# Kernel tuning notes

Hardware: AMD Instinct MI355X
Metric: run time of the kernel (lower is better)

## Reference

```python
import jax, jax.numpy as jnp
import numpy as np
from jax import lax

V, E, H, D = 50000, 300, 128, 128   # vocab, embed, gru_units, dense_units
B, S, W, T = 32, 512, 20, 16        # batch, sentences/doc, words/sentence, topics/doc


def setup_inputs() -> dict:
    key = jax.random.key(0)
    ks = jax.random.split(key, 16)
    word_ids = jax.random.randint(ks[0], (B, S, W), 0, V, dtype=jnp.int32)
    # contiguous equal topic segments, 1-based inclusive boundaries
    L = S // T
    starts = (1 + np.arange(T) * L).astype(np.int32)
    ends = (starts + L - 1).astype(np.int32)
    topic_start_ends = jnp.asarray(np.broadcast_to(np.stack([starts, ends], -1), (B, T, 2)))
    sc = 0.05
    def rn(k, shape, s=sc):
        return jax.random.normal(k, shape, dtype=jnp.float32) * s
    inp = {
        "word_ids": word_ids,
        "topic_start_ends": topic_start_ends,
        "emb": rn(ks[1], (V, E), 0.6),
        "Wih_f": rn(ks[2], (3 * H, E)), "Whh_f": rn(ks[3], (3 * H, H)),
        "bih_f": rn(ks[4], (3 * H,)),   "bhh_f": rn(ks[5], (3 * H,)),
        "Wih_b": rn(ks[6], (3 * H, E)), "Whh_b": rn(ks[7], (3 * H, H)),
        "bih_b": rn(ks[8], (3 * H,)),   "bhh_b": rn(ks[9], (3 * H,)),
        "W_att": rn(ks[10], (4 * H, 4 * H)), "v_att": rn(ks[11], (4 * H, 1)),
        "W1": rn(ks[12], (D, 4 * H)), "b1": rn(ks[13], (D,)),
        "W2": rn(ks[14], (1, D)),     "b2": rn(ks[15], (1,)),
    }
    return inp


def _gru_dir(x_sbe, Wih, Whh, bih, bhh, reverse):
    """x_sbe: [S,B,E] -> (outputs [S,B,H] in original time order, last hidden [B,H])."""
    h0 = jnp.zeros((x_sbe.shape[1], Whh.shape[1]), x_sbe.dtype)
    def step(h, xt):
        gx = xt @ Wih.T + bih            # [B,3H]
        gh = h @ Whh.T + bhh
        xr, xz, xn = jnp.split(gx, 3, axis=-1)   # PyTorch gate order: r,z,n
        hr, hz, hn = jnp.split(gh, 3, axis=-1)
        r = jax.nn.sigmoid(xr + hr)
        z = jax.nn.sigmoid(xz + hz)
        n = jnp.tanh(xn + r * hn)
        h2 = (1.0 - z) * n + z * h
        return h2, h2
    last, outs = lax.scan(step, h0, x_sbe, reverse=reverse)
    return outs, last


def reference(word_ids, topic_start_ends, emb,
              Wih_f, Whh_f, bih_f, bhh_f,
              Wih_b, Whh_b, bih_b, bhh_b,
              W_att, v_att, W1, b1, W2, b2):
    # --- sent_encoder: mean word embedding per sentence ---
    x = jnp.mean(emb[word_ids], axis=2)              # [B,S,E]
    # --- doc_encoder: biGRU over sentences ---
    xs = jnp.swapaxes(x, 0, 1)                       # [S,B,E]
    out_f, last_f = _gru_dir(xs, Wih_f, Whh_f, bih_f, bhh_f, reverse=False)
    out_b, last_b = _gru_dir(xs, Wih_b, Whh_b, bih_b, bhh_b, reverse=True)
    sent_rep = jnp.swapaxes(jnp.concatenate([out_f, out_b], axis=-1), 0, 1)  # [B,S,2H]
    # faithful to torch hidden.view(B, 2H) on [2,B,H] contiguous memory
    doc_vec = jnp.stack([last_f, last_b], axis=0).reshape(sent_rep.shape[0], 2 * last_f.shape[1])
    doc_rep = jnp.broadcast_to(doc_vec[:, None, :], sent_rep.shape)          # [B,S,2H]
    # --- topic segment extraction via boundary diffs on zero-padded GRU out ---
    Bn, Sn, twoH = sent_rep.shape
    Hn = twoH // 2
    P = jnp.pad(sent_rep, ((0, 0), (1, 1), (0, 0)))   # [B,S+2,2H]; index i = 1-based sentence i
    starts = topic_start_ends[..., 0]                 # [B,T], 1-based
    ends = topic_start_ends[..., 1]
    bidx = jnp.arange(Bn)[:, None]
    fw = P[bidx, ends, :Hn] - P[bidx, starts - 1, :Hn]      # forward-dir diff
    bw = P[bidx, starts, Hn:] - P[bidx, ends + 1, Hn:]      # backward-dir diff
    topic_mat = jnp.concatenate([fw, bw], axis=-1)          # [B,T,2H]
    # scatter: sentence s (0-based) belongs to topic with starts-1 <= s <= ends-1
    pos = jnp.arange(Sn, dtype=starts.dtype) + 1            # 1-based sentence ids
    seg = jax.vmap(lambda st: jnp.searchsorted(st, pos, side='right') - 1)(starts)  # [B,S]
    topic_rep = jnp.take_along_axis(topic_mat, seg[..., None], axis=1)              # [B,S,2H]
    # --- decoder ---
    cat_ds = jnp.concatenate([doc_rep, sent_rep], axis=-1)   # [B,S,4H]
    cat_ts = jnp.concatenate([topic_rep, sent_rep], axis=-1)
    doc_scores = jnp.tanh(cat_ds @ W_att) @ v_att            # [B,S,1]
    topic_scores = jnp.tanh(cat_ts @ W_att) @ v_att
    ssum = doc_scores + topic_scores
    context = (doc_scores / ssum) * doc_rep + (topic_scores / ssum) * topic_rep
    inp = jnp.concatenate([sent_rep, context], axis=-1)      # [B,S,4H]
    h = jax.nn.relu(inp @ W1.T + b1)                         # dropout = identity (eval)
    logits = h @ W2.T + b2                                   # [B,S,1]
    return logits
```

## Files before the change

kernel.cpp:

```cpp
#include <hip/hip_runtime.h>
#include <hip/hip_bf16.h>

#define B_ 32
#define S_ 512
#define W_ 20
#define T_ 16
#define E_ 300
#define H_ 128
#define M_ (B_*S_)

typedef float f32x4 __attribute__((ext_vector_type(4)));

#define OFF_GX        0ul
#define OFF_X         12582912ul
#define OFF_SENT      17498112ul
#define OFF_LASTF     21692416ul
#define OFF_LASTB     21696512ul
#define OFF_DOCVEC    21700608ul
#define OFF_TOPICMAT  21708800ul
#define OFF_DOCPART   21839872ul
#define OFF_TOPICPART 21856256ul
#define OFF_SEG       22118400ul
#define OFF_WTIH      22134784ul
#define OFF_BIASIH    22365184ul
#define OFF_W1T       22365952ul
#define OFF_H         22431488ul
#define OFF_SRPART    0ul
#define OFF_CTX       OFF_X

__global__ void prep_kernel(const float* __restrict__ Wih_f, const float* __restrict__ Wih_b,
                            const float* __restrict__ bih_f, const float* __restrict__ bih_b,
                            const float* __restrict__ W1,
                            float* __restrict__ Wt_ih, float* __restrict__ bias_ih,
                            float* __restrict__ W1t) {
  int idx = blockIdx.x * 256 + threadIdx.x;
  if (idx < E_ * 768) {
    int k = idx / 768, g = idx % 768;
    Wt_ih[idx] = (g < 384) ? Wih_f[g * E_ + k] : Wih_b[(g - 384) * E_ + k];
  }
  if (idx < 768) bias_ih[idx] = (idx < 384) ? bih_f[idx] : bih_b[idx - 384];
  if (idx < 512 * 128) { int k = idx / 128, j = idx % 128; W1t[idx] = W1[j * 512 + k]; }
}

__global__ void embed_mean_kernel(const int* __restrict__ wid, const float* __restrict__ emb,
                                  float* __restrict__ x) {
  int m = blockIdx.x;
  const int* ids = wid + (size_t)m * W_;
  int e = threadIdx.x;
  float s0 = 0.f, s1 = 0.f, s2 = 0.f;
  for (int w = 0; w < W_; w++) {
    const float* row = emb + (size_t)ids[w] * E_;
    s0 += row[e];
    s1 += row[e + 128];
    if (e < E_ - 256) s2 += row[e + 256];
  }
  const float inv = 1.0f / (float)W_;
  float* xr = x + (size_t)m * E_;
  xr[e] = s0 * inv; xr[e + 128] = s1 * inv; if (e < E_ - 256) xr[e + 256] = s2 * inv;
}

template<bool BIAS, bool ACCUM, bool RELU>
__global__ __launch_bounds__(256) void gemm64(
    const float* __restrict__ A, int lda,
    const float* __restrict__ B, int ldb,
    float* __restrict__ C, int ldc,
    const float* __restrict__ bias,
    int M, int N, int K) {
  __shared__ float As[16][68];
  __shared__ float Bs[16][68];
  const int tid = threadIdx.x;
  const int n0 = blockIdx.x * 64, m0 = blockIdx.y * 64;
  const int tx = tid & 15, ty = tid >> 4;
  const int am = tid >> 2, ak = (tid & 3) << 2;
  const int bk = tid >> 4, bn = (tid & 15) << 2;
  float acc[4][4] = {};
  for (int k0 = 0; k0 < K; k0 += 16) {
    float4 av = make_float4(0.f, 0.f, 0.f, 0.f);
    int arow = m0 + am;
    if (arow < M) {
      if (k0 + ak + 3 < K) {
        av = *(const float4*)(A + (size_t)arow * lda + k0 + ak);
      } else {
        float tmp[4] = {0.f, 0.f, 0.f, 0.f};
        #pragma unroll
        for (int i2 = 0; i2 < 4; i2++) { int k = k0 + ak + i2; if (k < K) tmp[i2] = A[(size_t)arow * lda + k]; }
        av = make_float4(tmp[0], tmp[1], tmp[2], tmp[3]);
      }
    }
    As[ak + 0][am] = av.x; As[ak + 1][am] = av.y; As[ak + 2][am] = av.z; As[ak + 3][am] = av.w;
    float4 bv = make_float4(0.f, 0.f, 0.f, 0.f);
    {
      int k = k0 + bk;
      if (k < K) bv = *(const float4*)(B + (size_t)k * ldb + n0 + bn);
    }
    *(float4*)&Bs[bk][bn] = bv;
    __syncthreads();
    #pragma unroll
    for (int kk = 0; kk < 16; kk++) {
      float4 a = *(const float4*)&As[kk][ty << 2];
      float4 b = *(const float4*)&Bs[kk][tx << 2];
      acc[0][0] = fmaf(a.x, b.x, acc[0][0]); acc[0][1] = fmaf(a.x, b.y, acc[0][1]);
      acc[0][2] = fmaf(a.x, b.z, acc[0][2]); acc[0][3] = fmaf(a.x, b.w, acc[0][3]);
      acc[1][0] = fmaf(a.y, b.x, acc[1][0]); acc[1][1] = fmaf(a.y, b.y, acc[1][1]);
      acc[1][2] = fmaf(a.y, b.z, acc[1][2]); acc[1][3] = fmaf(a.y, b.w, acc[1][3]);
      acc[2][0] = fmaf(a.z, b.x, acc[2][0]); acc[2][1] = fmaf(a.z, b.y, acc[2][1]);
      acc[2][2] = fmaf(a.z, b.z, acc[2][2]); acc[2][3] = fmaf(a.z, b.w, acc[2][3]);
      acc[3][0] = fmaf(a.w, b.x, acc[3][0]); acc[3][1] = fmaf(a.w, b.y, acc[3][1]);
      acc[3][2] = fmaf(a.w, b.z, acc[3][2]); acc[3][3] = fmaf(a.w, b.w, acc[3][3]);
    }
    __syncthreads();
  }
  float4 bias4 = make_float4(0.f, 0.f, 0.f, 0.f);
  if (BIAS) bias4 = *(const float4*)(bias + n0 + (tx << 2));
  #pragma unroll
  for (int i = 0; i < 4; i++) {
    int row = m0 + (ty << 2) + i;
    if (row >= M) break;
    float* cp = C + (size_t)row * ldc + n0 + (tx << 2);
    float4 v = make_float4(acc[i][0], acc[i][1], acc[i][2], acc[i][3]);
    if (BIAS) { v.x += bias4.x; v.y += bias4.y; v.z += bias4.z; v.w += bias4.w; }
    if (ACCUM) { float4 o = *(const float4*)cp; v.x += o.x; v.y += o.y; v.z += o.z; v.w += o.w; }
    if (RELU) { v.x = fmaxf(v.x, 0.f); v.y = fmaxf(v.y, 0.f); v.z = fmaxf(v.z, 0.f); v.w = fmaxf(v.w, 0.f); }
    *(float4*)cp = v;
  }
}

#define SWZ(k) ((k) + 4 * ((k) >> 4))

#define AW(N, V) asm volatile("v_accvgpr_write_b32 a" #N ", %0" :: "v"(V) : "a" #N)
#define AWQ(N0, N1, N2, N3, Q) do { AW(N0, (Q).x); AW(N1, (Q).y); AW(N2, (Q).z); AW(N3, (Q).w); } while (0)

#define A96CLOB \
  "a0","a1","a2","a3","a4","a5","a6","a7","a8","a9","a10","a11","a12","a13","a14","a15", \
  "a16","a17","a18","a19","a20","a21","a22","a23","a24","a25","a26","a27","a28","a29","a30","a31", \
  "a32","a33","a34","a35","a36","a37","a38","a39","a40","a41","a42","a43","a44","a45","a46","a47", \
  "a48","a49","a50","a51","a52","a53","a54","a55","a56","a57","a58","a59","a60","a61","a62","a63", \
  "a64","a65","a66","a67","a68","a69","a70","a71","a72","a73","a74","a75","a76","a77","a78","a79", \
  "a80","a81","a82","a83","a84","a85","a86","a87","a88","a89","a90","a91","a92","a93","a94","a95"

#define RD(T, N) "v_accvgpr_read_b32 %[" #T "], a" #N "\n\t"
#define FM(P, T, X) "v_fmac_f32 %[" #P "], %[" #T "], %[" #X "]\n\t"
#define COLA(CR, CZ, CN, X) \
  RD(t0, CR) RD(t1, CZ) RD(t2, CN) FM(pr, t0, X) FM(pz, t1, X) FM(pn, t2, X)

__global__ __launch_bounds__(512, 2) void gru_kernel(
    const float* __restrict__ gxbuf,
    const float* __restrict__ Whh_f, const float* __restrict__ Whh_b,
    const float* __restrict__ bhh_f, const float* __restrict__ bhh_b,
    float* __restrict__ sent_rep,
    float* __restrict__ last_f, float* __restrict__ last_b) {
  const int bid = blockIdx.x;
  const int dir = bid >> 5, b = bid & 31;
  const int t = threadIdx.x;
  const int j = t >> 2;
  const int q = t & 3;
  const int k0 = q << 5;
  const float* Whh = dir ? Whh_b : Whh_f;
  const float* bhh = dir ? bhh_b : bhh_f;

  {
    const float* Wr = Whh + (size_t)j * 128 + k0;
    const float* Wz = Whh + (size_t)(128 + j) * 128 + k0;
    const float* Wn = Whh + (size_t)(256 + j) * 128 + k0;
    f32x4 w0 = *(const f32x4*)(Wr + 0),  w1 = *(const f32x4*)(Wr + 4);
    f32x4 w2 = *(const f32x4*)(Wr + 8),  w3 = *(const f32x4*)(Wr + 12);
    f32x4 w4 = *(const f32x4*)(Wr + 16), w5 = *(const f32x4*)(Wr + 20);
    f32x4 w6 = *(const f32x4*)(Wr + 24), w7 = *(const f32x4*)(Wr + 28);
    AWQ(0, 1, 2, 3, w0);   AWQ(4, 5, 6, 7, w1);   AWQ(8, 9, 10, 11, w2);  AWQ(12, 13, 14, 15, w3);
    AWQ(16, 17, 18, 19, w4); AWQ(20, 21, 22, 23, w5); AWQ(24, 25, 26, 27, w6); AWQ(28, 29, 30, 31, w7);
    w0 = *(const f32x4*)(Wz + 0);  w1 = *(const f32x4*)(Wz + 4);
    w2 = *(const f32x4*)(Wz + 8);  w3 = *(const f32x4*)(Wz + 12);
    w4 = *(const f32x4*)(Wz + 16); w5 = *(const f32x4*)(Wz + 20);
    w6 = *(const f32x4*)(Wz + 24); w7 = *(const f32x4*)(Wz + 28);
    AWQ(32, 33, 34, 35, w0); AWQ(36, 37, 38, 39, w1); AWQ(40, 41, 42, 43, w2); AWQ(44, 45, 46, 47, w3);
    AWQ(48, 49, 50, 51, w4); AWQ(52, 53, 54, 55, w5); AWQ(56, 57, 58, 59, w6); AWQ(60, 61, 62, 63, w7);
    w0 = *(const f32x4*)(Wn + 0);  w1 = *(const f32x4*)(Wn + 4);
    w2 = *(const f32x4*)(Wn + 8);  w3 = *(const f32x4*)(Wn + 12);
    w4 = *(const f32x4*)(Wn + 16); w5 = *(const f32x4*)(Wn + 20);
    w6 = *(const f32x4*)(Wn + 24); w7 = *(const f32x4*)(Wn + 28);
    AWQ(64, 65, 66, 67, w0); AWQ(68, 69, 70, 71, w1); AWQ(72, 73, 74, 75, w2); AWQ(76, 77, 78, 79, w3);
    AWQ(80, 81, 82, 83, w4); AWQ(84, 85, 86, 87, w5); AWQ(88, 89, 90, 91, w6); AWQ(92, 93, 94, 95, w7);
  }

  const float cR = (q == 0) ? bhh[j] : 0.f;
  const float cZ = (q == 0) ? bhh[128 + j] : 0.f;
  const float cN = (q == 0) ? bhh[256 + j] : 0.f;
  const int gate = (q == 1) ? 0 : (q == 2) ? 1 : 2;
  const float mr = (q == 1) ? 1.f : 0.f;
  const float mz = (q == 2) ? 1.f : 0.f;

  __shared__ float lds[320];
  if (t < 128) lds[SWZ(t)] = 0.f;
  __syncthreads();

  const int stp = dir ? -1 : 1;
  const int ts0 = dir ? 511 : 0;
  const ptrdiff_t g768 = (ptrdiff_t)stp * 768;
  const ptrdiff_t s256 = (ptrdiff_t)stp * 256;
  const float* gq = gxbuf + (size_t)b * 512 * 768 + dir * 384 + gate * 128 + j + (size_t)ts0 * 768;
  float* sp = sent_rep + (size_t)b * 512 * 256 + dir * 128 + (size_t)ts0 * 256;
  float hprev = 0.f;
  float gx_c = gq[0];
  float gx_1 = gq[g768];

#define GRU_STEP(P, SOFF) do { \
    float gx_2 = 0.f; \
    if (s + 2 + (SOFF) < 512) gx_2 = gq[2 * g768]; \
    const f32x4* hv = (const f32x4*)(lds + (P) * 160 + 40 * q); \
    f32x4 h0 = hv[0], h1 = hv[1], h2 = hv[2], h3 = hv[3]; \
    f32x4 h4 = hv[5], h5 = hv[6], h6 = hv[7], h7 = hv[8]; \
    float pr = cR, pz = cZ, pn = cN; \
    { float t0v, t1v, t2v; \
      asm volatile( \
        COLA(0,32,64,x0)   COLA(1,33,65,x1)   COLA(2,34,66,x2)   COLA(3,35,67,x3) \
        COLA(4,36,68,x4)   COLA(5,37,69,x5)   COLA(6,38,70,x6)   COLA(7,39,71,x7) \
        COLA(8,40,72,x8)   COLA(9,41,73,x9)   COLA(10,42,74,x10) COLA(11,43,75,x11) \
        COLA(12,44,76,x12) COLA(13,45,77,x13) COLA(14,46,78,x14) COLA(15,47,79,x15) \
        : [pr]"+v"(pr), [pz]"+v"(pz), [pn]"+v"(pn), \
          [t0]"=&v"(t0v), [t1]"=&v"(t1v), [t2]"=&v"(t2v) \
        : [x0]"v"(h0.x), [x1]"v"(h0.y), [x2]"v"(h0.z), [x3]"v"(h0.w), \
          [x4]"v"(h1.x), [x5]"v"(h1.y), [x6]"v"(h1.z), [x7]"v"(h1.w), \
          [x8]"v"(h2.x), [x9]"v"(h2.y), [x10]"v"(h2.z), [x11]"v"(h2.w), \
          [x12]"v"(h3.x), [x13]"v"(h3.y), [x14]"v"(h3.z), [x15]"v"(h3.w) \
        : A96CLOB); \
      asm volatile( \
        COLA(16,48,80,x0)  COLA(17,49,81,x1)  COLA(18,50,82,x2)  COLA(19,51,83,x3) \
        COLA(20,52,84,x4)  COLA(21,53,85,x5)  COLA(22,54,86,x6)  COLA(23,55,87,x7) \
        COLA(24,56,88,x8)  COLA(25,57,89,x9)  COLA(26,58,90,x10) COLA(27,59,91,x11) \
        COLA(28,60,92,x12) COLA(29,61,93,x13) COLA(30,62,94,x14) COLA(31,63,95,x15) \
        : [pr]"+v"(pr), [pz]"+v"(pz), [pn]"+v"(pn), \
          [t0]"=&v"(t0v), [t1]"=&v"(t1v), [t2]"=&v"(t2v) \
        : [x0]"v"(h4.x), [x1]"v"(h4.y), [x2]"v"(h4.z), [x3]"v"(h4.w), \
          [x4]"v"(h5.x), [x5]"v"(h5.y), [x6]"v"(h5.z), [x7]"v"(h5.w), \
          [x8]"v"(h6.x), [x9]"v"(h6.y), [x10]"v"(h6.z), [x11]"v"(h6.w), \
          [x12]"v"(h7.x), [x13]"v"(h7.y), [x14]"v"(h7.z), [x15]"v"(h7.w) \
        : A96CLOB); } \
    pr = fmaf(mr, gx_c, pr); \
    pz = fmaf(mz, gx_c, pz); \
    pr += __shfl_xor(pr, 1); pr += __shfl_xor(pr, 2); \
    pz += __shfl_xor(pz, 1); pz += __shfl_xor(pz, 2); \
    pn += __shfl_xor(pn, 1); pn += __shfl_xor(pn, 2); \
    float xr = fminf(fmaxf(pr, -30.f), 30.f); \
    float xz = fminf(fmaxf(pz, -30.f), 30.f); \
    float r = 1.f / (1.f + __expf(-xr)); \
    float z = 1.f / (1.f + __expf(-xz)); \
    float xn = gx_c + r * pn; xn = fminf(fmaxf(xn, -15.f), 15.f); \
    float e2 = __expf(2.f * xn); \
    float n = (e2 - 1.f) / (e2 + 1.f); \
    float hnew = (1.f - z) * n + z * hprev; \
    hprev = hnew; \
    if (q == 0) { \
      lds[((P) ^ 1) * 160 + SWZ(j)] = hnew; \
      sp[j] = hnew; \
    } \
    __syncthreads(); \
    gq += g768; sp += s256; \
    gx_c = gx_1; gx_1 = gx_2; \
  } while (0)

  #pragma unroll 1
  for (int s = 0; s < 512; s += 2) {
    GRU_STEP(0, 0);
    GRU_STEP(1, 1);
  }
#undef GRU_STEP

  if (q == 0) (dir ? last_b : last_f)[b * 128 + j] = hprev;
}

__global__ void docvec_kernel(const float* __restrict__ last_f, const float* __restrict__ last_b,
                              float* __restrict__ doc_vec) {
  int idx = blockIdx.x * 256 + threadIdx.x;
  int i = idx >> 8, c = idx & 255;
  const float* src = (i < 16) ? last_f : last_b;
  int ii = (i < 16) ? i : i - 16;
  int bb = 2 * ii + (c >> 7);
  doc_vec[idx] = src[bb * 128 + (c & 127)];
}

__global__ void topicmat_kernel(const float* __restrict__ sent_rep, const int* __restrict__ tse,
                                float* __restrict__ topic_mat) {
  int bt = blockIdx.x;
  int b = bt >> 4, t = bt & 15;
  int st = tse[(b * 16 + t) * 2 + 0];
  int en = tse[(b * 16 + t) * 2 + 1];
  int jj = threadIdx.x;
  const float* sr = sent_rep + (size_t)b * 512 * 256;
  float val;
  if (jj < 128) {
    float a = sr[(size_t)(en - 1) * 256 + jj];
    float c = (st - 2 >= 0) ? sr[(size_t)(st - 2) * 256 + jj] : 0.f;
    val = a - c;
  } else {
    float a = sr[(size_t)(st - 1) * 256 + jj];
    float c = (en <= 511) ? sr[(size_t)en * 256 + jj] : 0.f;
    val = a - c;
  }
  topic_mat[(size_t)bt * 256 + jj] = val;
}

__global__ void seg_kernel(const int* __restrict__ tse, int* __restrict__ seg) {
  int idx = blockIdx.x * 256 + threadIdx.x;
  int b = idx >> 9, s = idx & 511;
  int pos = s + 1, cnt = 0;
  for (int t = 0; t < T_; t++) cnt += (tse[(b * T_ + t) * 2] <= pos);
  int sg = cnt - 1; sg = sg < 0 ? 0 : (sg > T_ - 1 ? T_ - 1 : sg);
  seg[idx] = sg;
}

__global__ void scores_ctx_kernel(const float* __restrict__ sr_part,
                                  const float* __restrict__ doc_part,
                                  const float* __restrict__ topic_part,
                                  const float* __restrict__ v_att,
                                  const float* __restrict__ doc_vec,
                                  const float* __restrict__ topic_mat,
                                  const int* __restrict__ seg,
                                  float* __restrict__ context) {
  int wid = threadIdx.x >> 6, lane = threadIdx.x & 63;
  int row = blockIdx.x * 4 + wid;
  int b = row >> 9;
  int sg = seg[row];
  const float* srp = sr_part + (size_t)row * 512;
  const float* dp = doc_part + (size_t)b * 512;
  const float* tp = topic_part + (size_t)(b * 16 + sg) * 512;
  float accd = 0.f, acct = 0.f;
  #pragma unroll
  for (int i = 0; i < 8; i++) {
    int n = lane + i * 64;
    float sp = srp[n], va = v_att[n];
    accd += tanhf(dp[n] + sp) * va;
    acct += tanhf(tp[n] + sp) * va;
  }
  #pragma unroll
  for (int off = 32; off; off >>= 1) { accd += __shfl_xor(accd, off); acct += __shfl_xor(acct, off); }
  float ssum = accd + acct;
  float rd = accd / ssum, rt = acct / ssum;
  const float* dv = doc_vec + (size_t)b * 256;
  const float* tm = topic_mat + (size_t)(b * 16 + sg) * 256;
  float* ctx = context + (size_t)row * 256;
  #pragma unroll
  for (int i = 0; i < 4; i++) {
    int jj = lane + i * 64;
    ctx[jj] = rd * dv[jj] + rt * tm[jj];
  }
}

__global__ void logits_kernel(const float* __restrict__ h, const float* __restrict__ W2,
                              const float* __restrict__ b2, float* __restrict__ out, int M) {
  int wid = threadIdx.x >> 6, lane = threadIdx.x & 63;
  int row = blockIdx.x * 4 + wid;
  if (row >= M) return;
  const float* hp = h + (size_t)row * 128;
  float s = hp[lane] * W2[lane] + hp[lane + 64] * W2[lane + 64];
  #pragma unroll
  for (int off = 32; off; off >>= 1) s += __shfl_xor(s, off);
  if (lane == 0) out[row] = s + b2[0];
}

extern "C" void kernel_launch(void* const* d_in, const int* in_sizes, int n_in,
                              void* d_out, int out_size, void* d_ws, size_t ws_size,
                              hipStream_t stream) {
  const int*   word_ids = (const int*)d_in[0];
  const int*   tse      = (const int*)d_in[1];
  const float* emb      = (const float*)d_in[2];
  const float* Wih_f    = (const float*)d_in[3];
  const float* Whh_f    = (const float*)d_in[4];
  const float* bih_f    = (const float*)d_in[5];
  const float* bhh_f    = (const float*)d_in[6];
  const float* Wih_b    = (const float*)d_in[7];
  const float* Whh_b    = (const float*)d_in[8];
  const float* bih_b    = (const float*)d_in[9];
  const float* bhh_b    = (const float*)d_in[10];
  const float* W_att    = (const float*)d_in[11];
  const float* v_att    = (const float*)d_in[12];
  const float* W1       = (const float*)d_in[13];
  const float* b1       = (const float*)d_in[14];
  const float* W2       = (const float*)d_in[15];
  const float* b2       = (const float*)d_in[16];
  float* ws  = (float*)d_ws;
  float* out = (float*)d_out;

  prep_kernel<<<900, 256, 0, stream>>>(Wih_f, Wih_b, bih_f, bih_b, W1,
                                       ws + OFF_WTIH, ws + OFF_BIASIH, ws + OFF_W1T);
  embed_mean_kernel<<<M_, 128, 0, stream>>>(word_ids, emb, ws + OFF_X);
  gemm64<true, false, false><<<dim3(12, 256), 256, 0, stream>>>(
      ws + OFF_X, E_, ws + OFF_WTIH, 768, ws + OFF_GX, 768, ws + OFF_BIASIH, M_, 768, E_);
  gru_kernel<<<64, 512, 0, stream>>>(ws + OFF_GX, Whh_f, Whh_b, bhh_f, bhh_b,
                                     ws + OFF_SENT, ws + OFF_LASTF, ws + OFF_LASTB);
  docvec_kernel<<<32, 256, 0, stream>>>(ws + OFF_LASTF, ws + OFF_LASTB, ws + OFF_DOCVEC);
  topicmat_kernel<<<512, 256, 0, stream>>>(ws + OFF_SENT, tse, ws + OFF_TOPICMAT);
  seg_kernel<<<64, 256, 0, stream>>>(tse, (int*)(ws + OFF_SEG));
  gemm64<false, false, false><<<dim3(8, 1), 256, 0, stream>>>(
      ws + OFF_DOCVEC, 256, W_att, 512, ws + OFF_DOCPART, 512, nullptr, 32, 512, 256);
  gemm64<false, false, false><<<dim3(8, 8), 256, 0, stream>>>(
      ws + OFF_TOPICMAT, 256, W_att, 512, ws + OFF_TOPICPART, 512, nullptr, 512, 512, 256);
  gemm64<false, false, false><<<dim3(8, 256), 256, 0, stream>>>(
      ws + OFF_SENT, 256, W_att + 256 * 512, 512, ws + OFF_SRPART, 512, nullptr, M_, 512, 256);
  scores_ctx_kernel<<<M_ / 4, 256, 0, stream>>>(
      ws + OFF_SRPART, ws + OFF_DOCPART, ws + OFF_TOPICPART, v_att,
      ws + OFF_DOCVEC, ws + OFF_TOPICMAT, (const int*)(ws + OFF_SEG), ws + OFF_CTX);
  gemm64<true, false, false><<<dim3(2, 256), 256, 0, stream>>>(
      ws + OFF_SENT, 256, ws + OFF_W1T, 128, ws + OFF_H, 128, b1, M_, 128, 256);
  gemm64<false, true, true><<<dim3(2, 256), 256, 0, stream>>>(
      ws + OFF_CTX, 256, ws + OFF_W1T + 256 * 128, 128, ws + OFF_H, 128, nullptr, M_, 128, 256);
  logits_kernel<<<M_ / 4, 256, 0, stream>>>(ws + OFF_H, W2, b2, out, M_);
}
```

Baseline: 771.1 us.

## Split GRU recurrent matvec across eight lanes per hidden unit

The recurrent GRU kernel now launches 1024 threads per block and assigns each hidden unit to 8 lanes instead of 4. Each lane therefore holds 16 columns of each gate's weights in AGPRs instead of 32, halving the serial FMA chain in every time step. The goal is to shorten the per-step latency of the sequential recurrence, which is the critical path of the whole pipeline. In exchange it adds a third shuffle-reduction stage, a block-wide barrier over 16 waves instead of 8, and changes the occupancy hints.

```diff
diff --git a/kernel.cpp b/kernel.cpp
--- a/kernel.cpp
+++ b/kernel.cpp
@@ -130,20 +130,18 @@
 #define AW(N, V) asm volatile("v_accvgpr_write_b32 a" #N ", %0" :: "v"(V) : "a" #N)
 #define AWQ(N0, N1, N2, N3, Q) do { AW(N0, (Q).x); AW(N1, (Q).y); AW(N2, (Q).z); AW(N3, (Q).w); } while (0)
 
-#define A96CLOB \
+#define A48CLOB \
   "a0","a1","a2","a3","a4","a5","a6","a7","a8","a9","a10","a11","a12","a13","a14","a15", \
   "a16","a17","a18","a19","a20","a21","a22","a23","a24","a25","a26","a27","a28","a29","a30","a31", \
-  "a32","a33","a34","a35","a36","a37","a38","a39","a40","a41","a42","a43","a44","a45","a46","a47", \
-  "a48","a49","a50","a51","a52","a53","a54","a55","a56","a57","a58","a59","a60","a61","a62","a63", \
-  "a64","a65","a66","a67","a68","a69","a70","a71","a72","a73","a74","a75","a76","a77","a78","a79", \
-  "a80","a81","a82","a83","a84","a85","a86","a87","a88","a89","a90","a91","a92","a93","a94","a95"
+  "a32","a33","a34","a35","a36","a37","a38","a39","a40","a41","a42","a43","a44","a45","a46","a47"
 
 #define RD(T, N) "v_accvgpr_read_b32 %[" #T "], a" #N "\n\t"
 #define FM(P, T, X) "v_fmac_f32 %[" #P "], %[" #T "], %[" #X "]\n\t"
 #define COLA(CR, CZ, CN, X) \
   RD(t0, CR) RD(t1, CZ) RD(t2, CN) FM(pr, t0, X) FM(pz, t1, X) FM(pn, t2, X)
 
-__global__ __launch_bounds__(512, 2) void gru_kernel(
+__global__ __launch_bounds__(1024) __attribute__((amdgpu_waves_per_eu(4, 4)))
+void gru_kernel(
     const float* __restrict__ gxbuf,
     const float* __restrict__ Whh_f, const float* __restrict__ Whh_b,
     const float* __restrict__ bhh_f, const float* __restrict__ bhh_b,
@@ -152,9 +150,9 @@
   const int bid = blockIdx.x;
   const int dir = bid >> 5, b = bid & 31;
   const int t = threadIdx.x;
-  const int j = t >> 2;
-  const int q = t & 3;
-  const int k0 = q << 5;
+  const int j = t >> 3;
+  const int q = t & 7;
+  const int k0 = q << 4;
   const float* Whh = dir ? Whh_b : Whh_f;
   const float* bhh = dir ? bhh_b : bhh_f;
 
@@ -164,22 +162,13 @@
     const float* Wn = Whh + (size_t)(256 + j) * 128 + k0;
     f32x4 w0 = *(const f32x4*)(Wr + 0),  w1 = *(const f32x4*)(Wr + 4);
     f32x4 w2 = *(const f32x4*)(Wr + 8),  w3 = *(const f32x4*)(Wr + 12);
-    f32x4 w4 = *(const f32x4*)(Wr + 16), w5 = *(const f32x4*)(Wr + 20);
-    f32x4 w6 = *(const f32x4*)(Wr + 24), w7 = *(const f32x4*)(Wr + 28);
     AWQ(0, 1, 2, 3, w0);   AWQ(4, 5, 6, 7, w1);   AWQ(8, 9, 10, 11, w2);  AWQ(12, 13, 14, 15, w3);
-    AWQ(16, 17, 18, 19, w4); AWQ(20, 21, 22, 23, w5); AWQ(24, 25, 26, 27, w6); AWQ(28, 29, 30, 31, w7);
     w0 = *(const f32x4*)(Wz + 0);  w1 = *(const f32x4*)(Wz + 4);
     w2 = *(const f32x4*)(Wz + 8);  w3 = *(const f32x4*)(Wz + 12);
-    w4 = *(const f32x4*)(Wz + 16); w5 = *(const f32x4*)(Wz + 20);
-    w6 = *(const f32x4*)(Wz + 24); w7 = *(const f32x4*)(Wz + 28);
-    AWQ(32, 33, 34, 35, w0); AWQ(36, 37, 38, 39, w1); AWQ(40, 41, 42, 43, w2); AWQ(44, 45, 46, 47, w3);
-    AWQ(48, 49, 50, 51, w4); AWQ(52, 53, 54, 55, w5); AWQ(56, 57, 58, 59, w6); AWQ(60, 61, 62, 63, w7);
+    AWQ(16, 17, 18, 19, w0); AWQ(20, 21, 22, 23, w1); AWQ(24, 25, 26, 27, w2); AWQ(28, 29, 30, 31, w3);
     w0 = *(const f32x4*)(Wn + 0);  w1 = *(const f32x4*)(Wn + 4);
     w2 = *(const f32x4*)(Wn + 8);  w3 = *(const f32x4*)(Wn + 12);
-    w4 = *(const f32x4*)(Wn + 16); w5 = *(const f32x4*)(Wn + 20);
-    w6 = *(const f32x4*)(Wn + 24); w7 = *(const f32x4*)(Wn + 28);
-    AWQ(64, 65, 66, 67, w0); AWQ(68, 69, 70, 71, w1); AWQ(72, 73, 74, 75, w2); AWQ(76, 77, 78, 79, w3);
-    AWQ(80, 81, 82, 83, w4); AWQ(84, 85, 86, 87, w5); AWQ(88, 89, 90, 91, w6); AWQ(92, 93, 94, 95, w7);
+    AWQ(32, 33, 34, 35, w0); AWQ(36, 37, 38, 39, w1); AWQ(40, 41, 42, 43, w2); AWQ(44, 45, 46, 47, w3);
   }
 
   const float cR = (q == 0) ? bhh[j] : 0.f;
@@ -206,40 +195,27 @@
 #define GRU_STEP(P, SOFF) do { \
     float gx_2 = 0.f; \
     if (s + 2 + (SOFF) < 512) gx_2 = gq[2 * g768]; \
-    const f32x4* hv = (const f32x4*)(lds + (P) * 160 + 40 * q); \
+    const f32x4* hv = (const f32x4*)(lds + (P) * 160 + 20 * q); \
     f32x4 h0 = hv[0], h1 = hv[1], h2 = hv[2], h3 = hv[3]; \
-    f32x4 h4 = hv[5], h5 = hv[6], h6 = hv[7], h7 = hv[8]; \
     float pr = cR, pz = cZ, pn = cN; \
     { float t0v, t1v, t2v; \
       asm volatile( \
-        COLA(0,32,64,x0)   COLA(1,33,65,x1)   COLA(2,34,66,x2)   COLA(3,35,67,x3) \
-        COLA(4,36,68,x4)   COLA(5,37,69,x5)   COLA(6,38,70,x6)   COLA(7,39,71,x7) \
-        COLA(8,40,72,x8)   COLA(9,41,73,x9)   COLA(10,42,74,x10) COLA(11,43,75,x11) \
-        COLA(12,44,76,x12) COLA(13,45,77,x13) COLA(14,46,78,x14) COLA(15,47,79,x15) \
+        COLA(0,16,32,x0)   COLA(1,17,33,x1)   COLA(2,18,34,x2)   COLA(3,19,35,x3) \
+        COLA(4,20,36,x4)   COLA(5,21,37,x5)   COLA(6,22,38,x6)   COLA(7,23,39,x7) \
+        COLA(8,24,40,x8)   COLA(9,25,41,x9)   COLA(10,26,42,x10) COLA(11,27,43,x11) \
+        COLA(12,28,44,x12) COLA(13,29,45,x13) COLA(14,30,46,x14) COLA(15,31,47,x15) \
         : [pr]"+v"(pr), [pz]"+v"(pz), [pn]"+v"(pn), \
           [t0]"=&v"(t0v), [t1]"=&v"(t1v), [t2]"=&v"(t2v) \
         : [x0]"v"(h0.x), [x1]"v"(h0.y), [x2]"v"(h0.z), [x3]"v"(h0.w), \
           [x4]"v"(h1.x), [x5]"v"(h1.y), [x6]"v"(h1.z), [x7]"v"(h1.w), \
           [x8]"v"(h2.x), [x9]"v"(h2.y), [x10]"v"(h2.z), [x11]"v"(h2.w), \
           [x12]"v"(h3.x), [x13]"v"(h3.y), [x14]"v"(h3.z), [x15]"v"(h3.w) \
-        : A96CLOB); \
-      asm volatile( \
-        COLA(16,48,80,x0)  COLA(17,49,81,x1)  COLA(18,50,82,x2)  COLA(19,51,83,x3) \
-        COLA(20,52,84,x4)  COLA(21,53,85,x5)  COLA(22,54,86,x6)  COLA(23,55,87,x7) \
-        COLA(24,56,88,x8)  COLA(25,57,89,x9)  COLA(26,58,90,x10) COLA(27,59,91,x11) \
-        COLA(28,60,92,x12) COLA(29,61,93,x13) COLA(30,62,94,x14) COLA(31,63,95,x15) \
-        : [pr]"+v"(pr), [pz]"+v"(pz), [pn]"+v"(pn), \
-          [t0]"=&v"(t0v), [t1]"=&v"(t1v), [t2]"=&v"(t2v) \
-        : [x0]"v"(h4.x), [x1]"v"(h4.y), [x2]"v"(h4.z), [x3]"v"(h4.w), \
-          [x4]"v"(h5.x), [x5]"v"(h5.y), [x6]"v"(h5.z), [x7]"v"(h5.w), \
-          [x8]"v"(h6.x), [x9]"v"(h6.y), [x10]"v"(h6.z), [x11]"v"(h6.w), \
-          [x12]"v"(h7.x), [x13]"v"(h7.y), [x14]"v"(h7.z), [x15]"v"(h7.w) \
-        : A96CLOB); } \
+        : A48CLOB); } \
     pr = fmaf(mr, gx_c, pr); \
     pz = fmaf(mz, gx_c, pz); \
-    pr += __shfl_xor(pr, 1); pr += __shfl_xor(pr, 2); \
-    pz += __shfl_xor(pz, 1); pz += __shfl_xor(pz, 2); \
-    pn += __shfl_xor(pn, 1); pn += __shfl_xor(pn, 2); \
+    pr += __shfl_xor(pr, 1); pr += __shfl_xor(pr, 2); pr += __shfl_xor(pr, 4); \
+    pz += __shfl_xor(pz, 1); pz += __shfl_xor(pz, 2); pz += __shfl_xor(pz, 4); \
+    pn += __shfl_xor(pn, 1); pn += __shfl_xor(pn, 2); pn += __shfl_xor(pn, 4); \
     float xr = fminf(fmaxf(pr, -30.f), 30.f); \
     float xz = fminf(fmaxf(pz, -30.f), 30.f); \
     float r = 1.f / (1.f + __expf(-xr)); \
@@ -385,8 +361,8 @@
   embed_mean_kernel<<<M_, 128, 0, stream>>>(word_ids, emb, ws + OFF_X);
   gemm64<true, false, false><<<dim3(12, 256), 256, 0, stream>>>(
       ws + OFF_X, E_, ws + OFF_WTIH, 768, ws + OFF_GX, 768, ws + OFF_BIASIH, M_, 768, E_);
-  gru_kernel<<<64, 512, 0, stream>>>(ws + OFF_GX, Whh_f, Whh_b, bhh_f, bhh_b,
-                                     ws + OFF_SENT, ws + OFF_LASTF, ws + OFF_LASTB);
+  gru_kernel<<<64, 1024, 0, stream>>>(ws + OFF_GX, Whh_f, Whh_b, bhh_f, bhh_b,
+                                      ws + OFF_SENT, ws + OFF_LASTF, ws + OFF_LASTB);
   docvec_kernel<<<32, 256, 0, stream>>>(ws + OFF_LASTF, ws + OFF_LASTB, ws + OFF_DOCVEC);
   topicmat_kernel<<<512, 256, 0, stream>>>(ws + OFF_SENT, tse, ws + OFF_TOPICMAT);
   seg_kernel<<<64, 256, 0, stream>>>(tse, (int*)(ws + OFF_SEG));
```

New measurement: 849.1 us. 10.1% more time.
